# Performance work log

Measured on AMD Instinct MI355X. Metric: run time of the kernel, lower is better.

Reference implementation:

```python
import jax, jax.numpy as jnp
import numpy as np

B, T, D = 2, 2048, 1024
N_HEADS, D_HEAD, WINDOW = 16, 64, 256
SCALE = D_HEAD ** -0.5


def setup_inputs() -> dict:
    key = jax.random.key(0)
    k1, k2, k3 = jax.random.split(key, 3)
    x = jax.random.normal(k1, (B, T, D), dtype=jnp.float32)
    # torch Linear weights are [out_features, in_features], init std=0.02
    w_qkv = jax.random.normal(k2, (3 * N_HEADS * D_HEAD, D), dtype=jnp.float32) * 0.02
    w_out = jax.random.normal(k3, (D, N_HEADS * D_HEAD), dtype=jnp.float32) * 0.02
    return {"x": x, "w_qkv": w_qkv, "w_out": w_out}


def reference(x, w_qkv, w_out):
    b, t, d = x.shape
    qkv = jnp.einsum('btd,ed->bte', x, w_qkv)  # [B,T,3*H*Dh]
    q, k, v = jnp.split(qkv, 3, axis=-1)
    def heads(u):
        return u.reshape(b, t, N_HEADS, D_HEAD).transpose(0, 2, 1, 3)  # [B,H,T,Dh]
    q, k, v = heads(q), heads(k), heads(v)
    scores = jnp.einsum('bhqd,bhkd->bhqk', q, k) * SCALE  # [B,H,T,T]
    pos = jnp.arange(t)
    dist = pos[:, None] - pos[None, :]  # query - key
    allowed = (dist >= 0) & (dist < WINDOW)  # causal sliding window
    neg_inf = jnp.asarray(-jnp.inf, dtype=scores.dtype)
    scores = jnp.where(allowed[None, None], scores, neg_inf)
    attn = jax.nn.softmax(scores, axis=-1)
    out = jnp.einsum('bhqk,bhkd->bhqd', attn, v)  # [B,H,T,Dh]
    out = out.transpose(0, 2, 1, 3).reshape(b, t, N_HEADS * D_HEAD)
    return jnp.einsum('bte,de->btd', out, w_out)
```

## Files before the change

### kernel.cpp

```cpp
#include <hip/hip_runtime.h>
#include <hip/hip_bf16.h>

typedef unsigned short bfu;
typedef __attribute__((ext_vector_type(8))) short short8;
typedef __attribute__((ext_vector_type(4))) float floatx4;
typedef __attribute__((ext_vector_type(2))) __fp16 fp16x2;
typedef __attribute__((ext_vector_type(4))) _Float16 half4v;

#define B_ 2
#define T_ 2048
#define D_ 1024
#define NH 16
#define DH 64
#define WIN 256
#define QKV_COLS 3072
#define NX  (B_ * T_ * D_)
#define NWQ (QKV_COLS * D_)
#define NWO (D_ * D_)

__device__ __forceinline__ bfu f2b_bits(float f) {
  union { __hip_bfloat16 h; bfu u; } cv;
  cv.h = __float2bfloat16(f);
  return cv.u;
}

__device__ __forceinline__ void gl_lds16(const bfu* g, bfu* l) {
  __builtin_amdgcn_global_load_lds(
      (const __attribute__((address_space(1))) unsigned int*)g,
      (__attribute__((address_space(3))) unsigned int*)l, 16, 0, 0);
}

#define BARRIER() __builtin_amdgcn_s_barrier()

__global__ void cvt3_kernel(const float* __restrict__ x, const float* __restrict__ wq,
                            const float* __restrict__ wo, bfu* __restrict__ out) {
  int i = (blockIdx.x * 256 + threadIdx.x) * 4;
  const float* src;
  int off;
  if (i < NX)            { src = x;  off = 0; }
  else if (i < NX + NWQ) { src = wq; off = NX; }
  else                   { src = wo; off = NX + NWQ; }
  floatx4 v = *(const floatx4*)(src + (i - off));
  out[i + 0] = f2b_bits(v.x);
  out[i + 1] = f2b_bits(v.y);
  out[i + 2] = f2b_bits(v.z);
  out[i + 3] = f2b_bits(v.w);
}

template <int EPI, int TN>
__global__ __launch_bounds__(256) void gemm_bt_kernel(const bfu* __restrict__ A,
                                                      const bfu* __restrict__ Bm,
                                                      void* __restrict__ C,
                                                      int M, int N, int K) {
  constexpr int NJ = TN / 32;
  __shared__ __align__(16) bfu As[128][64];
  __shared__ __align__(16) bfu Bs[TN][64];
  const int tid = threadIdx.x;
  const int wave = tid >> 6, lane = tid & 63;
  const int quad = lane >> 4, cl = lane & 15;
  const int lr = lane >> 3, lg = lane & 7, sg = lg ^ lr;
  const int wm = (wave >> 1) * 64, wn = (wave & 1) * (TN / 2);
  const int m0 = blockIdx.y * 128, n0 = blockIdx.x * TN;

  floatx4 acc[4][NJ] = {};

  for (int k0 = 0; k0 < K; k0 += 64) {
    __syncthreads();
#pragma unroll
    for (int i = 0; i < 4; ++i) {
      const int row = i * 32 + wave * 8;
      gl_lds16(A + (size_t)(m0 + row + lr) * K + k0 + sg * 8, &As[row][0]);
    }
#pragma unroll
    for (int i = 0; i < TN / 32; ++i) {
      const int row = i * 32 + wave * 8;
      gl_lds16(Bm + (size_t)(n0 + row + lr) * K + k0 + sg * 8, &Bs[row][0]);
    }
    __syncthreads();
#pragma unroll
    for (int ks = 0; ks < 2; ++ks) {
      const int gsw = ks * 4 + quad;
      short8 af[4], bfr[NJ];
#pragma unroll
      for (int im = 0; im < 4; ++im)
        af[im] = *(const short8*)(&As[wm + im * 16 + cl][(gsw ^ (cl & 7)) << 3]);
#pragma unroll
      for (int in = 0; in < NJ; ++in)
        bfr[in] = *(const short8*)(&Bs[wn + in * 16 + cl][(gsw ^ (cl & 7)) << 3]);
#pragma unroll
      for (int im = 0; im < 4; ++im)
#pragma unroll
        for (int in = 0; in < NJ; ++in)
          acc[im][in] = __builtin_amdgcn_mfma_f32_16x16x32_bf16(af[im], bfr[in], acc[im][in], 0, 0, 0);
    }
  }
  const float qs = (EPI == 2 && n0 < 1024) ? 0.125f : 1.0f;
  const bool vf16 = (EPI == 2) && (n0 >= 2048);
#pragma unroll
  for (int im = 0; im < 4; ++im) {
#pragma unroll
    for (int r = 0; r < 4; ++r) {
      const size_t row = (size_t)(m0 + wm + im * 16 + quad * 4 + r);
#pragma unroll
      for (int in = 0; in < NJ; ++in) {
        const size_t idx = row * (size_t)N + (n0 + wn + in * 16 + cl);
        const float val = acc[im][in][r];
        if constexpr (EPI == 0) {
          ((float*)C)[idx] = val;
        } else {
          bfu bits;
          if (vf16) { union { _Float16 h; bfu u; } cv; cv.h = (_Float16)val; bits = cv.u; }
          else      { bits = f2b_bits(val * qs); }
          ((bfu*)C)[idx] = bits;
        }
      }
    }
  }
}

__global__ __launch_bounds__(512, 2) void gemm8p_qkv_kernel(const bfu* __restrict__ A,
                                                            const bfu* __restrict__ Bm,
                                                            bfu* __restrict__ C,
                                                            int M, int N, int K) {
  __shared__ __align__(16) bfu As[2][256][64];
  __shared__ __align__(16) bfu Bs[2][192][64];
  const int tid = threadIdx.x;
  const int wave = tid >> 6, lane = tid & 63;
  const int quad = lane >> 4, cl = lane & 15;
  const int lr = lane >> 3, lg = lane & 7, sg = lg ^ lr;

  const int cpx = gridDim.x >> 3;
  const int swz = (blockIdx.x & 7) * cpx + (blockIdx.x >> 3);
  const int m0 = (swz >> 4) * 256, n0 = (swz & 15) * 192;
  const int wmRow = (wave >> 2) * 128;
  const int wnCol = (wave & 3) * 48;

  floatx4 acc[2][4][3] = {};
  const int NT = K >> 6;

  auto stageA = [&](int buf, int r0, int k0s) {
    gl_lds16(A + (size_t)(m0 + r0 + lr) * K + k0s + sg * 8, &As[buf][r0][0]);
  };
  auto stageB = [&](int buf, int r0, int k0s) {
    gl_lds16(Bm + (size_t)(n0 + r0 + lr) * K + k0s + sg * 8, &Bs[buf][r0][0]);
  };
  const int a0 = wave * 8;
  const int bc0 = wave * 24;

  auto ldA = [&](int buf, int rbase, int ks) -> short8 {
    return *(const short8*)(&As[buf][rbase + cl][((ks * 4 + quad) ^ (cl & 7)) << 3]);
  };
  auto ldB = [&](int buf, int rbase, int ks) -> short8 {
    return *(const short8*)(&Bs[buf][rbase + cl][((ks * 4 + quad) ^ (cl & 7)) << 3]);
  };

  stageA(0, a0, 0);        stageA(0, 128 + a0, 0);
  stageB(0, bc0, 0);       stageB(0, bc0 + 8, 0);   stageB(0, bc0 + 16, 0);
  stageA(0, 64 + a0, 0);   stageA(0, 192 + a0, 0);
  asm volatile("s_waitcnt vmcnt(2)");
  BARRIER();

  for (int t = 0; t < NT; ++t) {
    const int cur = t & 1, nxt = cur ^ 1;
    const int kn = (t + 1) << 6;
    const bool pf = (t + 1 < NT);
    short8 af[4][2], bfv[3][2];

#pragma unroll
    for (int ks = 0; ks < 2; ++ks) {
#pragma unroll
      for (int im = 0; im < 4; ++im) af[im][ks] = ldA(cur, wmRow + im * 16, ks);
#pragma unroll
      for (int nf = 0; nf < 3; ++nf) bfv[nf][ks] = ldB(cur, wnCol + nf * 16, ks);
    }
    if (pf) {
      stageA(nxt, a0, kn);      stageA(nxt, 128 + a0, kn);
      stageB(nxt, bc0, kn);     stageB(nxt, bc0 + 8, kn);  stageB(nxt, bc0 + 16, kn);
    }
    __builtin_amdgcn_s_setprio(1);
#pragma unroll
    for (int ks = 0; ks < 2; ++ks)
#pragma unroll
      for (int im = 0; im < 4; ++im)
#pragma unroll
        for (int nf = 0; nf < 3; ++nf)
          acc[0][im][nf] = __builtin_amdgcn_mfma_f32_16x16x32_bf16(af[im][ks], bfv[nf][ks], acc[0][im][nf], 0, 0, 0);
    __builtin_amdgcn_s_setprio(0);
    if (pf) asm volatile("s_waitcnt vmcnt(5)");
    else    asm volatile("s_waitcnt vmcnt(0)");
    BARRIER();

#pragma unroll
    for (int ks = 0; ks < 2; ++ks)
#pragma unroll
      for (int im = 0; im < 4; ++im) af[im][ks] = ldA(cur, wmRow + 64 + im * 16, ks);
    if (pf) {
      stageA(nxt, 64 + a0, kn); stageA(nxt, 192 + a0, kn);
    }
    __builtin_amdgcn_s_setprio(1);
#pragma unroll
    for (int ks = 0; ks < 2; ++ks)
#pragma unroll
      for (int im = 0; im < 4; ++im)
#pragma unroll
        for (int nf = 0; nf < 3; ++nf)
          acc[1][im][nf] = __builtin_amdgcn_mfma_f32_16x16x32_bf16(af[im][ks], bfv[nf][ks], acc[1][im][nf], 0, 0, 0);
    __builtin_amdgcn_s_setprio(0);
    if (pf) asm volatile("s_waitcnt vmcnt(2)");
    BARRIER();
  }

#pragma unroll
  for (int qm = 0; qm < 2; ++qm) {
#pragma unroll
    for (int im = 0; im < 4; ++im) {
#pragma unroll
      for (int r = 0; r < 4; ++r) {
        const size_t row = (size_t)(m0 + wmRow + qm * 64 + im * 16 + quad * 4 + r);
#pragma unroll
        for (int nf = 0; nf < 3; ++nf) {
          const int colb = n0 + wnCol + nf * 16;
          const float qs = (colb < 1024) ? 0.125f : 1.0f;
          const bool vf16 = (colb >= 2048);
          const size_t idx = row * (size_t)N + colb + cl;
          const float val = acc[qm][im][nf][r];
          bfu bits;
          if (vf16) { union { _Float16 h; bfu u; } cv; cv.h = (_Float16)val; bits = cv.u; }
          else      { bits = f2b_bits(val * qs); }
          C[idx] = bits;
        }
      }
    }
  }
}

__global__ __launch_bounds__(512, 4) void swa_kernel(const bfu* __restrict__ qkv,
                                                     bfu* __restrict__ aout) {
  __shared__ __align__(16) bfu Qs[128][64];
  __shared__ __align__(16) bfu Ks[2][64][64];
  __shared__ __align__(16) bfu Vs[2][64][64];

  const int qt = blockIdx.x, h = blockIdx.y, b = blockIdx.z;
  const int tid = threadIdx.x, wave = tid >> 6, lane = tid & 63;
  const int quad = lane >> 4, cl = lane & 15;
  const int lr = lane >> 3, lg = lane & 7, sg = lg ^ lr;
  const int q0 = qt * 128;
  const bfu* qb = qkv + (size_t)b * T_ * QKV_COLS + h * DH;
  const bfu* kb = qb + 1024;
  const bfu* vb = qb + 2048;

  const int jt0 = (qt >= 2) ? 2 * qt - 4 : 0;
  const int njt = (2 * qt + 1) - jt0 + 1;

  const int vrow = tid >> 3;
  const int vcol = (tid & 7) * 8;

#pragma unroll
  for (int i = 0; i < 2; ++i) {
    const int row = wave * 16 + i * 8;
    gl_lds16(qb + (size_t)(q0 + row + lr) * QKV_COLS + sg * 8, &Qs[row][0]);
  }
  gl_lds16(kb + (size_t)(jt0 * 64 + wave * 8 + lr) * QKV_COLS + sg * 8, &Ks[0][wave * 8][0]);
  {
    union { short8 v; bfu u[8]; } t0;
    t0.v = *(const short8*)(vb + (size_t)(jt0 * 64 + vrow) * QKV_COLS + vcol);
#pragma unroll
    for (int e = 0; e < 8; ++e) {
      const int d = vcol + e;
      const int gp = ((vrow >> 2) + d + (d >> 3)) & 15;
      Vs[0][d][gp * 4 + (vrow & 3)] = t0.u[e];
    }
  }
  __syncthreads();

  float l_acc = 0.f;
  floatx4 acc[4] = {};
  const int ddc = cl + (cl >> 3);
  const int qw0 = q0 + wave * 16;

  for (int it = 0; it < njt; ++it) {
    const int cur = it & 1, nxt = cur ^ 1;
    const int k0 = (jt0 + it) * 64;
    const bool pf = (it + 1 < njt);

    union { short8 v; bfu u[8]; } vp;
    if (pf) {
      const int kn = k0 + 64;
      gl_lds16(kb + (size_t)(kn + wave * 8 + lr) * QKV_COLS + sg * 8, &Ks[nxt][wave * 8][0]);
      vp.v = *(const short8*)(vb + (size_t)(kn + vrow) * QKV_COLS + vcol);
    }

    bool live[4];
#pragma unroll
    for (int jk = 0; jk < 4; ++jk) {
      const int kg0 = k0 + jk * 16;
      live[jk] = (qw0 + 15 >= kg0) && (qw0 <= kg0 + 270);
    }

    floatx4 s[4] = {};
#pragma unroll
    for (int ks = 0; ks < 2; ++ks) {
      const int col = ((ks * 4 + quad) ^ (cl & 7)) << 3;
      short8 bq = *(const short8*)(&Qs[wave * 16 + cl][col]);
#pragma unroll
      for (int jk = 0; jk < 4; ++jk)
        if (live[jk]) {
          short8 ak = *(const short8*)(&Ks[cur][jk * 16 + cl][col]);
          s[jk] = __builtin_amdgcn_mfma_f32_16x16x32_bf16(ak, bq, s[jk], 0, 0, 0);
        }
    }

    const int qg = qw0 + cl;
    half4v af[4] = {};
#pragma unroll
    for (int jk = 0; jk < 4; ++jk) {
      if (!live[jk]) continue;
      float p[4];
#pragma unroll
      for (int r = 0; r < 4; ++r) {
        const int kg = k0 + jk * 16 + quad * 4 + r;
        const int dist = qg - kg;
        p[r] = (dist >= 0 && dist < WIN) ? __expf(s[jk][r]) : 0.f;
        l_acc += p[r];
      }
      union { fp16x2 h2[2]; half4v h4; } u;
      u.h2[0] = __builtin_amdgcn_cvt_pkrtz(p[0], p[1]);
      u.h2[1] = __builtin_amdgcn_cvt_pkrtz(p[2], p[3]);
      af[jk] = u.h4;
    }

#pragma unroll
    for (int kt = 0; kt < 4; ++kt) {
      if (!live[kt]) continue;
#pragma unroll
      for (int jd = 0; jd < 4; ++jd) {
        const int d = jd * 16 + cl;
        const int gp = (kt * 4 + quad + ddc + jd * 2) & 15;
        half4v bv = *(const half4v*)(&Vs[cur][d][gp * 4]);
        acc[jd] = __builtin_amdgcn_mfma_f32_16x16x16f16(af[kt], bv, acc[jd], 0, 0, 0);
      }
    }

    if (pf) {
#pragma unroll
      for (int e = 0; e < 8; ++e) {
        const int d = vcol + e;
        const int gp = ((vrow >> 2) + d + (d >> 3)) & 15;
        Vs[nxt][d][gp * 4 + (vrow & 3)] = vp.u[e];
      }
    }
    __syncthreads();
  }

  l_acc += __shfl_xor(l_acc, 16);
  l_acc += __shfl_xor(l_acc, 32);
  const float linv = 1.f / l_acc;
  float lq[4];
#pragma unroll
  for (int r = 0; r < 4; ++r) lq[r] = __shfl(linv, quad * 4 + r);

  bfu* ob = aout + (size_t)b * T_ * D_ + h * DH;
#pragma unroll
  for (int r = 0; r < 4; ++r) {
    const size_t row = (size_t)(q0 + wave * 16 + quad * 4 + r);
#pragma unroll
    for (int jd = 0; jd < 4; ++jd)
      ob[row * D_ + jd * 16 + cl] = f2b_bits(acc[jd][r] * lq[r]);
  }
}

extern "C" void kernel_launch(void* const* d_in, const int* in_sizes, int n_in,
                              void* d_out, int out_size, void* d_ws, size_t ws_size,
                              hipStream_t stream) {
  const float* x     = (const float*)d_in[0];
  const float* w_qkv = (const float*)d_in[1];
  const float* w_out = (const float*)d_in[2];
  float* out = (float*)d_out;
  char* ws = (char*)d_ws;

  bfu* xb    = (bfu*)(ws);
  bfu* wqkvb = (bfu*)(ws + (8ull << 20));
  bfu* woutb = (bfu*)(ws + (14ull << 20));
  bfu* qkvb  = (bfu*)(ws + (16ull << 20));
  bfu* attb  = (bfu*)(ws + (40ull << 20));

  cvt3_kernel<<<(NX + NWQ + NWO) / 1024, 256, 0, stream>>>(x, w_qkv, w_out, xb);

  gemm8p_qkv_kernel<<<dim3(256), 512, 0, stream>>>(xb, wqkvb, qkvb, B_ * T_, QKV_COLS, D_);

  swa_kernel<<<dim3(T_ / 128, NH, B_), 512, 0, stream>>>(qkvb, attb);

  gemm_bt_kernel<0, 64><<<dim3(D_ / 64, (B_ * T_) / 128), 256, 0, stream>>>(
      attb, woutb, out, B_ * T_, D_, D_);
}
```

Measured before the change: 145.3 us.

## Replace output projection GEMM with double-buffered 256x64-tile pipelined kernel

Replaces the simple single-buffered 128x64 output-projection GEMM with a 512-thread kernel using 256x64 tiles and double-buffered LDS. It prefetches the next K tile while computing, uses split waitcnt/barrier phases, raises wave priority around the MFMA blocks and swizzles block order. The aim is to hide global-to-LDS latency and cut per-iteration sync stalls. In exchange the grid is smaller (256 blocks), which may leave some CUs underused.

```diff
diff --git a/kernel.cpp b/kernel.cpp
--- a/kernel.cpp
+++ b/kernel.cpp
@@ -47,77 +47,6 @@
   out[i + 3] = f2b_bits(v.w);
 }
 
-template <int EPI, int TN>
-__global__ __launch_bounds__(256) void gemm_bt_kernel(const bfu* __restrict__ A,
-                                                      const bfu* __restrict__ Bm,
-                                                      void* __restrict__ C,
-                                                      int M, int N, int K) {
-  constexpr int NJ = TN / 32;
-  __shared__ __align__(16) bfu As[128][64];
-  __shared__ __align__(16) bfu Bs[TN][64];
-  const int tid = threadIdx.x;
-  const int wave = tid >> 6, lane = tid & 63;
-  const int quad = lane >> 4, cl = lane & 15;
-  const int lr = lane >> 3, lg = lane & 7, sg = lg ^ lr;
-  const int wm = (wave >> 1) * 64, wn = (wave & 1) * (TN / 2);
-  const int m0 = blockIdx.y * 128, n0 = blockIdx.x * TN;
-
-  floatx4 acc[4][NJ] = {};
-
-  for (int k0 = 0; k0 < K; k0 += 64) {
-    __syncthreads();
-#pragma unroll
-    for (int i = 0; i < 4; ++i) {
-      const int row = i * 32 + wave * 8;
-      gl_lds16(A + (size_t)(m0 + row + lr) * K + k0 + sg * 8, &As[row][0]);
-    }
-#pragma unroll
-    for (int i = 0; i < TN / 32; ++i) {
-      const int row = i * 32 + wave * 8;
-      gl_lds16(Bm + (size_t)(n0 + row + lr) * K + k0 + sg * 8, &Bs[row][0]);
-    }
-    __syncthreads();
-#pragma unroll
-    for (int ks = 0; ks < 2; ++ks) {
-      const int gsw = ks * 4 + quad;
-      short8 af[4], bfr[NJ];
-#pragma unroll
-      for (int im = 0; im < 4; ++im)
-        af[im] = *(const short8*)(&As[wm + im * 16 + cl][(gsw ^ (cl & 7)) << 3]);
-#pragma unroll
-      for (int in = 0; in < NJ; ++in)
-        bfr[in] = *(const short8*)(&Bs[wn + in * 16 + cl][(gsw ^ (cl & 7)) << 3]);
-#pragma unroll
-      for (int im = 0; im < 4; ++im)
-#pragma unroll
-        for (int in = 0; in < NJ; ++in)
-          acc[im][in] = __builtin_amdgcn_mfma_f32_16x16x32_bf16(af[im], bfr[in], acc[im][in], 0, 0, 0);
-    }
-  }
-  const float qs = (EPI == 2 && n0 < 1024) ? 0.125f : 1.0f;
-  const bool vf16 = (EPI == 2) && (n0 >= 2048);
-#pragma unroll
-  for (int im = 0; im < 4; ++im) {
-#pragma unroll
-    for (int r = 0; r < 4; ++r) {
-      const size_t row = (size_t)(m0 + wm + im * 16 + quad * 4 + r);
-#pragma unroll
-      for (int in = 0; in < NJ; ++in) {
-        const size_t idx = row * (size_t)N + (n0 + wn + in * 16 + cl);
-        const float val = acc[im][in][r];
-        if constexpr (EPI == 0) {
-          ((float*)C)[idx] = val;
-        } else {
-          bfu bits;
-          if (vf16) { union { _Float16 h; bfu u; } cv; cv.h = (_Float16)val; bits = cv.u; }
-          else      { bits = f2b_bits(val * qs); }
-          ((bfu*)C)[idx] = bits;
-        }
-      }
-    }
-  }
-}
-
 __global__ __launch_bounds__(512, 2) void gemm8p_qkv_kernel(const bfu* __restrict__ A,
                                                             const bfu* __restrict__ Bm,
                                                             bfu* __restrict__ C,
@@ -234,6 +163,106 @@
   }
 }
 
+__global__ __launch_bounds__(512, 2) void gemm2p_out_kernel(const bfu* __restrict__ A,
+                                                            const bfu* __restrict__ Bm,
+                                                            float* __restrict__ C,
+                                                            int M, int N, int K) {
+  __shared__ __align__(16) bfu As[2][256][64];
+  __shared__ __align__(16) bfu Bs[2][64][64];
+  const int tid = threadIdx.x;
+  const int wave = tid >> 6, lane = tid & 63;
+  const int quad = lane >> 4, cl = lane & 15;
+  const int lr = lane >> 3, lg = lane & 7, sg = lg ^ lr;
+
+  const int cpx = gridDim.x >> 3;
+  const int swz = (blockIdx.x & 7) * cpx + (blockIdx.x >> 3);
+  const int m0 = (swz >> 4) * 256, n0 = (swz & 15) * 64;
+  const int wmRow = (wave >> 2) * 128;
+  const int wnCol = (wave & 3) * 16;
+
+  floatx4 acc[2][4] = {};
+  const int NT = K >> 6;
+
+  auto stageA = [&](int buf, int r0, int k0s) {
+    gl_lds16(A + (size_t)(m0 + r0 + lr) * K + k0s + sg * 8, &As[buf][r0][0]);
+  };
+  auto stageB = [&](int buf, int r0, int k0s) {
+    gl_lds16(Bm + (size_t)(n0 + r0 + lr) * K + k0s + sg * 8, &Bs[buf][r0][0]);
+  };
+  const int a0 = wave * 8;
+  const int bc0 = wave * 8;
+
+  auto ldA = [&](int buf, int rbase, int ks) -> short8 {
+    return *(const short8*)(&As[buf][rbase + cl][((ks * 4 + quad) ^ (cl & 7)) << 3]);
+  };
+  auto ldB = [&](int buf, int rbase, int ks) -> short8 {
+    return *(const short8*)(&Bs[buf][rbase + cl][((ks * 4 + quad) ^ (cl & 7)) << 3]);
+  };
+
+  stageA(0, a0, 0);        stageA(0, 128 + a0, 0);
+  stageB(0, bc0, 0);
+  stageA(0, 64 + a0, 0);   stageA(0, 192 + a0, 0);
+  asm volatile("s_waitcnt vmcnt(2)");
+  BARRIER();
+
+  for (int t = 0; t < NT; ++t) {
+    const int cur = t & 1, nxt = cur ^ 1;
+    const int kn = (t + 1) << 6;
+    const bool pf = (t + 1 < NT);
+    short8 af[4][2], bfv[2];
+
+#pragma unroll
+    for (int ks = 0; ks < 2; ++ks) {
+#pragma unroll
+      for (int im = 0; im < 4; ++im) af[im][ks] = ldA(cur, wmRow + im * 16, ks);
+      bfv[ks] = ldB(cur, wnCol, ks);
+    }
+    if (pf) {
+      stageA(nxt, a0, kn);  stageA(nxt, 128 + a0, kn);
+      stageB(nxt, bc0, kn);
+    }
+    __builtin_amdgcn_s_setprio(1);
+#pragma unroll
+    for (int ks = 0; ks < 2; ++ks)
+#pragma unroll
+      for (int im = 0; im < 4; ++im)
+        acc[0][im] = __builtin_amdgcn_mfma_f32_16x16x32_bf16(af[im][ks], bfv[ks], acc[0][im], 0, 0, 0);
+    __builtin_amdgcn_s_setprio(0);
+    if (pf) asm volatile("s_waitcnt vmcnt(3)");
+    else    asm volatile("s_waitcnt vmcnt(0)");
+    BARRIER();
+
+#pragma unroll
+    for (int ks = 0; ks < 2; ++ks)
+#pragma unroll
+      for (int im = 0; im < 4; ++im) af[im][ks] = ldA(cur, wmRow + 64 + im * 16, ks);
+    if (pf) {
+      stageA(nxt, 64 + a0, kn); stageA(nxt, 192 + a0, kn);
+    }
+    __builtin_amdgcn_s_setprio(1);
+#pragma unroll
+    for (int ks = 0; ks < 2; ++ks)
+#pragma unroll
+      for (int im = 0; im < 4; ++im)
+        acc[1][im] = __builtin_amdgcn_mfma_f32_16x16x32_bf16(af[im][ks], bfv[ks], acc[1][im], 0, 0, 0);
+    __builtin_amdgcn_s_setprio(0);
+    if (pf) asm volatile("s_waitcnt vmcnt(2)");
+    BARRIER();
+  }
+
+#pragma unroll
+  for (int qm = 0; qm < 2; ++qm) {
+#pragma unroll
+    for (int im = 0; im < 4; ++im) {
+#pragma unroll
+      for (int r = 0; r < 4; ++r) {
+        const size_t row = (size_t)(m0 + wmRow + qm * 64 + im * 16 + quad * 4 + r);
+        C[row * (size_t)N + n0 + wnCol + cl] = acc[qm][im][r];
+      }
+    }
+  }
+}
+
 __global__ __launch_bounds__(512, 4) void swa_kernel(const bfu* __restrict__ qkv,
                                                      bfu* __restrict__ aout) {
   __shared__ __align__(16) bfu Qs[128][64];
@@ -390,6 +419,5 @@
 
   swa_kernel<<<dim3(T_ / 128, NH, B_), 512, 0, stream>>>(qkvb, attb);
 
-  gemm_bt_kernel<0, 64><<<dim3(D_ / 64, (B_ * T_) / 128), 256, 0, stream>>>(
-      attb, woutb, out, B_ * T_, D_, D_);
-}
+  gemm2p_out_kernel<<<dim3(256), 512, 0, stream>>>(attb, woutb, out, B_ * T_, D_, D_);
+}
```

New measurement: 145.7 us. Within noise of the previous version (+0.3%).
